# Performance work log

Measured on AMD Instinct MI355X. Metric: run time of the kernel, lower is better.

The kernel has to match this reference:

```python
import jax, jax.numpy as jnp
import numpy as np

HIDDEN = 300
INPUT_DIM = 300


def setup_inputs() -> dict:
    key = jax.random.key(0)
    k_in, k_wih, k_whh, k_bih, k_bhh = jax.random.split(key, 5)
    bound = 1.0 / np.sqrt(HIDDEN)  # PyTorch RNNCell init: U(-1/sqrt(H), 1/sqrt(H))
    inputs = jax.random.normal(k_in, (512, 512, INPUT_DIM), dtype=jnp.float32)
    W_ih = jax.random.uniform(k_wih, (HIDDEN, INPUT_DIM), jnp.float32, -bound, bound)
    W_hh = jax.random.uniform(k_whh, (HIDDEN, HIDDEN), jnp.float32, -bound, bound)
    b_ih = jax.random.uniform(k_bih, (HIDDEN,), jnp.float32, -bound, bound)
    b_hh = jax.random.uniform(k_bhh, (HIDDEN,), jnp.float32, -bound, bound)
    return {"inputs": inputs, "W_ih": W_ih, "W_hh": W_hh, "b_ih": b_ih, "b_hh": b_hh}


def reference(inputs, W_ih, W_hh, b_ih, b_hh):
    # inputs: [seq, batch, input_dim]; vanilla tanh RNNCell scanned over time.
    seq, bz, _ = inputs.shape
    # Precompute input projections for all timesteps in one big GEMM.
    x_proj = jnp.einsum('sbi,hi->sbh', inputs, W_ih) + b_ih + b_hh  # [seq, batch, H]

    def step(ht, xp):
        ht = jnp.tanh(xp + ht @ W_hh.T)
        return ht, None

    h0 = jnp.zeros((bz, HIDDEN), dtype=inputs.dtype)
    ht, _ = jax.lax.scan(step, h0, x_proj)
    return ht
```

## Files before the change

### kernel.cpp

```cpp
#include <hip/hip_runtime.h>
#include <hip/hip_bf16.h>


typedef unsigned short u16;
typedef unsigned int   u32;
typedef __attribute__((ext_vector_type(8)))  short bf16x8;
typedef __attribute__((ext_vector_type(4)))  short s16x4;
typedef __attribute__((ext_vector_type(4)))  float f32x4;
typedef __attribute__((ext_vector_type(16))) float f32x16;
typedef __attribute__((ext_vector_type(2)))  unsigned int u32x2;
typedef __attribute__((ext_vector_type(4)))  unsigned int u32x4;

#define HID 300
#define KP  320
#define SEQ 512
#define BZ  512
#define MTOT (SEQ*BZ)

__device__ __forceinline__ u16 f2bf(float f) {
    u32 u = __float_as_uint(f);
    return (u16)((u + 0x7FFFu + ((u >> 16) & 1u)) >> 16);
}
__device__ __forceinline__ float bf2f(u16 h) {
    return __uint_as_float((u32)h << 16);
}
__device__ __forceinline__ float tanh_fast(float x) {
    float e = __builtin_amdgcn_exp2f(x * 2.8853900817779268f);
    float r = __builtin_amdgcn_rcpf(e + 1.0f);
    return __builtin_fmaf(-2.0f, r, 1.0f);
}
__device__ __forceinline__ u32 pack2(float a, float b) {
    __hip_bfloat162 t = __float22bfloat162_rn(float2{a, b});
    return *(u32*)&t;
}
__device__ __forceinline__ void lds_barrier() {
    asm volatile("s_waitcnt lgkmcnt(0)\n\ts_barrier" ::: "memory");
}

__global__ void prep_kernel(const float* __restrict__ wih,
                            const float* __restrict__ whh,
                            const float* __restrict__ bih,
                            const float* __restrict__ bhh,
                            u16* __restrict__ wihp, u16* __restrict__ whhp,
                            float* __restrict__ bias) {
    int n = blockIdx.x, k = threadIdx.x;
    bool v = (n < HID) && (k < HID);
    int src = n * HID + k, dst = n * KP + k;
    wihp[dst] = v ? f2bf(wih[src]) : (u16)0;
    whhp[dst] = v ? f2bf(whh[src]) : (u16)0;
    if (k == 0) bias[n] = (n < HID) ? (bih[n] + bhh[n]) : 0.0f;
}

__global__ __launch_bounds__(512, 1) void xproj_kernel(
    const float* __restrict__ in, const u16* __restrict__ wihp,
    const float* __restrict__ bias, u16* __restrict__ xp) {
    __shared__ __align__(16) u16 As[2][4096];
    __shared__ __align__(16) u16 Bs[2][10240];

    const int tid = threadIdx.x;
    const int w = tid >> 6, l = tid & 63;
    const int mi = w & 3, ni = w >> 2;
    const int l31 = l & 31, l5 = l >> 5;
    const int m0 = blockIdx.x * 128;

    const int sm = tid >> 2, skg = tid & 3;

    f32x16 acc[5];
#pragma unroll
    for (int j = 0; j < 5; ++j)
#pragma unroll
        for (int r = 0; r < 16; ++r) acc[j][r] = 0.0f;

    auto loadA = [&](int it, f32x4& v0, f32x4& v1) {
        int gk = it * 32 + skg * 8;
        const float* p = in + (size_t)(m0 + sm) * HID + gk;
        if (gk <= 292) { v0 = *(const f32x4*)p; v1 = *(const f32x4*)(p + 4); }
        else if (gk <= 296) { v0 = *(const f32x4*)p; v1 = f32x4{0.f,0.f,0.f,0.f}; }
        else { v0 = f32x4{0.f,0.f,0.f,0.f}; v1 = f32x4{0.f,0.f,0.f,0.f}; }
    };
    auto writeA = [&](int buf, const f32x4& v0, const f32x4& v1) {
        u32x4 pk;
        pk[0] = pack2(v0[0], v0[1]); pk[1] = pack2(v0[2], v0[3]);
        pk[2] = pack2(v1[0], v1[1]); pk[3] = pack2(v1[2], v1[3]);
        *(u32x4*)&As[buf][(skg >> 1) * 2048 + sm * 16 + (skg & 1) * 8] = pk;
    };
    auto stageB = [&](int buf, int it) {
#pragma unroll
        for (int s = 0; s < 3; ++s) {
            int i = w + 8 * s;
            if (i < 20) {
                int c = i & 3, ng = i >> 2;
                int n = ng * 64 + l;
                const u16* g = wihp + n * KP + it * 32 + c * 8;
                u16* d = &Bs[buf][c * 2560 + ng * 512];
                __builtin_amdgcn_global_load_lds(
                    (const __attribute__((address_space(1))) void*)g,
                    (__attribute__((address_space(3))) void*)d, 16, 0, 0);
            }
        }
    };

    {
        f32x4 v0, v1;
        loadA(0, v0, v1);
        writeA(0, v0, v1);
        stageB(0, 0);
    }
    __syncthreads();

#pragma unroll 1
    for (int it = 0; it < 10; ++it) {
        const int cb = it & 1, nb = (it + 1) & 1;
        f32x4 v0, v1;
        if (it < 9) {
            loadA(it + 1, v0, v1);
            stageB(nb, it + 1);
        }
#pragma unroll
        for (int s = 0; s < 2; ++s) {
            bf16x8 a = *(const bf16x8*)&As[cb][s * 2048 + mi * 512 + l31 * 16 + l5 * 8];
#pragma unroll
            for (int j = 0; j < 5; ++j) {
                bf16x8 b = *(const bf16x8*)&Bs[cb][(s * 2 + l5) * 2560 + ((ni * 5 + j) * 32 + l31) * 8];
                acc[j] = __builtin_amdgcn_mfma_f32_32x32x16_bf16(a, b, acc[j], 0, 0, 0);
            }
        }
        if (it < 9) writeA(nb, v0, v1);
        __syncthreads();
    }

    const int mbase = m0 + mi * 32;
#pragma unroll
    for (int j = 0; j < 5; ++j) {
        int n = (ni * 5 + j) * 32 + l31;
        if (n < HID) {
            float bs = bias[n];
#pragma unroll
            for (int reg = 0; reg < 16; ++reg) {
                int row = (reg & 3) + 8 * (reg >> 2) + 4 * l5;
                xp[(size_t)(mbase + row) * HID + n] = f2bf(acc[j][reg] + bs);
            }
        }
    }
}

__global__ __launch_bounds__(512, 2) void rnn_recur_kernel(
    const u16* __restrict__ xp, const u16* __restrict__ whhp,
    float* __restrict__ out) {
    __shared__ __align__(16) u16 hb[2][16 * 328];

    const int tid = threadIdx.x;
    const int w = tid >> 6;
    const int l = tid & 63;
    const int br = l & 15;
    const int q  = l >> 4;
    const int b0 = blockIdx.x * 16;
    const bool t3 = (w < 4);

    for (int i = tid; i < (2 * 16 * 328) / 2; i += 512) ((u32*)hb)[i] = 0;

    bf16x8 Af[3][10];
#pragma unroll
    for (int j = 0; j < 3; ++j) {
        if (j < 2 || t3) {
            const int nt = w + 8 * j;
            const u16* wrow = whhp + (size_t)(nt * 16 + br) * KP;
#pragma unroll
            for (int ks = 0; ks < 10; ++ks)
                Af[j][ks] = *(const bf16x8*)(wrow + ks * 32 + q * 8);
        }
    }
#pragma unroll
    for (int j = 0; j < 3; ++j)
        if (j < 2 || t3)
#pragma unroll
            for (int ks = 0; ks < 10; ++ks)
                asm volatile("" : "+a"(Af[j][ks]));

    int xo[3];
#pragma unroll
    for (int j = 0; j < 3; ++j) {
        int n0 = (w + 8 * j) * 16 + q * 4;
        xo[j] = (n0 < HID && (j < 2 || t3)) ? ((b0 + br) * HID + n0) : -1;
    }

    const s16x4 z4 = {0, 0, 0, 0};
    s16x4 xc[3], xn[3];
#pragma unroll
    for (int j = 0; j < 3; ++j) {
        xc[j] = (xo[j] >= 0) ? *(const s16x4*)(xp + xo[j]) : z4;
        xn[j] = (xo[j] >= 0) ? *(const s16x4*)(xp + (size_t)BZ * HID + xo[j]) : z4;
    }

    lds_barrier();

#pragma unroll 1
    for (int t = 0; t < SEQ; ++t) {
        const u16* hc = hb[t & 1];
        u16*       hn = hb[(t + 1) & 1];

        s16x4 xf[3];
        {
            int t2 = (t + 2 < SEQ) ? (t + 2) : (SEQ - 1);
            const u16* base = xp + (size_t)t2 * (BZ * HID);
#pragma unroll
            for (int j = 0; j < 3; ++j)
                xf[j] = (xo[j] >= 0) ? *(const s16x4*)(base + xo[j]) : z4;
        }

        f32x4 a0, a1, a2;
#pragma unroll
        for (int r = 0; r < 4; ++r) { a0[r] = 0.f; a1[r] = 0.f; a2[r] = 0.f; }

#pragma unroll
        for (int ks = 0; ks < 10; ++ks) {
            bf16x8 bfr = *(const bf16x8*)&hc[br * 328 + ks * 32 + q * 8];
            a0 = __builtin_amdgcn_mfma_f32_16x16x32_bf16(Af[0][ks], bfr, a0, 0, 0, 0);
            a1 = __builtin_amdgcn_mfma_f32_16x16x32_bf16(Af[1][ks], bfr, a1, 0, 0, 0);
            if (t3)
                a2 = __builtin_amdgcn_mfma_f32_16x16x32_bf16(Af[2][ks], bfr, a2, 0, 0, 0);
        }

        {
            int n0 = w * 16 + q * 4;
            u32x2 pk;
            pk[0] = pack2(tanh_fast(a0[0] + bf2f((u16)xc[0][0])),
                          tanh_fast(a0[1] + bf2f((u16)xc[0][1])));
            pk[1] = pack2(tanh_fast(a0[2] + bf2f((u16)xc[0][2])),
                          tanh_fast(a0[3] + bf2f((u16)xc[0][3])));
            *(u32x2*)&hn[br * 328 + n0] = pk;
        }
        {
            int n0 = (w + 8) * 16 + q * 4;
            u32x2 pk;
            pk[0] = pack2(tanh_fast(a1[0] + bf2f((u16)xc[1][0])),
                          tanh_fast(a1[1] + bf2f((u16)xc[1][1])));
            pk[1] = pack2(tanh_fast(a1[2] + bf2f((u16)xc[1][2])),
                          tanh_fast(a1[3] + bf2f((u16)xc[1][3])));
            *(u32x2*)&hn[br * 328 + n0] = pk;
        }
        if (t3) {
            int n0 = (w + 16) * 16 + q * 4;
            u32x2 pk;
            pk[0] = pack2(tanh_fast(a2[0] + bf2f((u16)xc[2][0])),
                          tanh_fast(a2[1] + bf2f((u16)xc[2][1])));
            pk[1] = pack2(tanh_fast(a2[2] + bf2f((u16)xc[2][2])),
                          tanh_fast(a2[3] + bf2f((u16)xc[2][3])));
            *(u32x2*)&hn[br * 328 + n0] = pk;
        }
        lds_barrier();

#pragma unroll
        for (int j = 0; j < 3; ++j) { xc[j] = xn[j]; xn[j] = xf[j]; }
    }

    const u16* hf = hb[0];
    for (int i = tid; i < 16 * HID; i += 512) {
        int r = i / HID, n = i - r * HID;
        out[(size_t)(b0 + r) * HID + n] = bf2f(hf[r * 328 + n]);
    }
}

extern "C" void kernel_launch(void* const* d_in, const int* in_sizes, int n_in,
                              void* d_out, int out_size, void* d_ws, size_t ws_size,
                              hipStream_t stream) {
    const float* in  = (const float*)d_in[0];
    const float* wih = (const float*)d_in[1];
    const float* whh = (const float*)d_in[2];
    const float* bih = (const float*)d_in[3];
    const float* bhh = (const float*)d_in[4];

    char* ws = (char*)d_ws;
    const size_t XP_BYTES = (size_t)MTOT * HID * sizeof(u16);
    u16*   xpb  = (u16*)ws;
    u16*   wihp = (u16*)(ws + XP_BYTES);
    u16*   whhp = (u16*)(ws + XP_BYTES + (size_t)KP * KP * 2);
    float* bias = (float*)(ws + XP_BYTES + 2 * (size_t)KP * KP * 2);

    prep_kernel<<<KP, KP, 0, stream>>>(wih, whh, bih, bhh, wihp, whhp, bias);
    xproj_kernel<<<MTOT / 128, 512, 0, stream>>>(in, wihp, bias, xpb);
    rnn_recur_kernel<<<BZ / 16, 512, 0, stream>>>(xpb, whhp, (float*)d_out);
}
```

Before: 1.091 ms.

## Use 4 waves per block in RNN recurrence with 5 tiles per wave

The recurrent kernel now runs 256 threads (4 waves) per block, and each wave owns 5 output column tiles instead of 2-3. This balances work across waves and makes the per-step barrier cheaper. The accumulators are seeded with the precomputed input projection, which removes the separate add before tanh. The h fragments are loaded once into registers and reused over two MFMA phases, so the first two tiles' tanh and store can overlap the remaining MFMAs. In exchange, each wave has a longer serial chain of MFMAs per timestep and holds more weight fragments in AGPRs.

Result: slower. 1.285 ms (+17.7%).

```diff
diff --git a/kernel.cpp b/kernel.cpp
--- a/kernel.cpp
+++ b/kernel.cpp
@@ -24,8 +24,8 @@
 __device__ __forceinline__ float bf2f(u16 h) {
     return __uint_as_float((u32)h << 16);
 }
-__device__ __forceinline__ float tanh_fast(float x) {
-    float e = __builtin_amdgcn_exp2f(x * 2.8853900817779268f);
+__device__ __forceinline__ float tanh_fast(float y) {
+    float e = __builtin_amdgcn_exp2f(y * 2.8853900817779268f);
     float r = __builtin_amdgcn_rcpf(e + 1.0f);
     return __builtin_fmaf(-2.0f, r, 1.0f);
 }
@@ -144,7 +144,7 @@
     }
 }
 
-__global__ __launch_bounds__(512, 2) void rnn_recur_kernel(
+__global__ __launch_bounds__(256, 1) void rnn_recur_kernel(
     const u16* __restrict__ xp, const u16* __restrict__ whhp,
     float* __restrict__ out) {
     __shared__ __align__(16) u16 hb[2][16 * 328];
@@ -155,39 +155,35 @@
     const int br = l & 15;
     const int q  = l >> 4;
     const int b0 = blockIdx.x * 16;
-    const bool t3 = (w < 4);
-
-    for (int i = tid; i < (2 * 16 * 328) / 2; i += 512) ((u32*)hb)[i] = 0;
-
-    bf16x8 Af[3][10];
-#pragma unroll
-    for (int j = 0; j < 3; ++j) {
-        if (j < 2 || t3) {
-            const int nt = w + 8 * j;
-            const u16* wrow = whhp + (size_t)(nt * 16 + br) * KP;
-#pragma unroll
-            for (int ks = 0; ks < 10; ++ks)
-                Af[j][ks] = *(const bf16x8*)(wrow + ks * 32 + q * 8);
-        }
-    }
-#pragma unroll
-    for (int j = 0; j < 3; ++j)
-        if (j < 2 || t3)
-#pragma unroll
-            for (int ks = 0; ks < 10; ++ks)
-                asm volatile("" : "+a"(Af[j][ks]));
-
-    int xo[3];
-#pragma unroll
-    for (int j = 0; j < 3; ++j) {
-        int n0 = (w + 8 * j) * 16 + q * 4;
-        xo[j] = (n0 < HID && (j < 2 || t3)) ? ((b0 + br) * HID + n0) : -1;
+
+    for (int i = tid; i < (2 * 16 * 328) / 2; i += 256) ((u32*)hb)[i] = 0;
+
+    bf16x8 Af[5][10];
+#pragma unroll
+    for (int j = 0; j < 5; ++j) {
+        const int nt = w + 4 * j;
+        const u16* wrow = whhp + (size_t)(nt * 16 + br) * KP;
+#pragma unroll
+        for (int ks = 0; ks < 10; ++ks)
+            Af[j][ks] = *(const bf16x8*)(wrow + ks * 32 + q * 8);
+    }
+#pragma unroll
+    for (int j = 0; j < 5; ++j)
+#pragma unroll
+        for (int ks = 0; ks < 10; ++ks)
+            asm volatile("" : "+a"(Af[j][ks]));
+
+    int xo[5];
+#pragma unroll
+    for (int j = 0; j < 5; ++j) {
+        int n0 = (w + 4 * j) * 16 + q * 4;
+        xo[j] = (n0 < HID) ? ((b0 + br) * HID + n0) : -1;
     }
 
     const s16x4 z4 = {0, 0, 0, 0};
-    s16x4 xc[3], xn[3];
-#pragma unroll
-    for (int j = 0; j < 3; ++j) {
+    s16x4 xc[5], xn[5];
+#pragma unroll
+    for (int j = 0; j < 5; ++j) {
         xc[j] = (xo[j] >= 0) ? *(const s16x4*)(xp + xo[j]) : z4;
         xn[j] = (xo[j] >= 0) ? *(const s16x4*)(xp + (size_t)BZ * HID + xo[j]) : z4;
     }
@@ -199,63 +195,63 @@
         const u16* hc = hb[t & 1];
         u16*       hn = hb[(t + 1) & 1];
 
-        s16x4 xf[3];
+        s16x4 xf[5];
         {
             int t2 = (t + 2 < SEQ) ? (t + 2) : (SEQ - 1);
             const u16* base = xp + (size_t)t2 * (BZ * HID);
 #pragma unroll
-            for (int j = 0; j < 3; ++j)
+            for (int j = 0; j < 5; ++j)
                 xf[j] = (xo[j] >= 0) ? *(const s16x4*)(base + xo[j]) : z4;
         }
 
-        f32x4 a0, a1, a2;
-#pragma unroll
-        for (int r = 0; r < 4; ++r) { a0[r] = 0.f; a1[r] = 0.f; a2[r] = 0.f; }
-
+        f32x4 a[5];
+#pragma unroll
+        for (int j = 0; j < 5; ++j)
+#pragma unroll
+            for (int r = 0; r < 4; ++r)
+                a[j][r] = bf2f((u16)xc[j][r]);
+
+        bf16x8 bfr[10];
 #pragma unroll
         for (int ks = 0; ks < 10; ++ks) {
-            bf16x8 bfr = *(const bf16x8*)&hc[br * 328 + ks * 32 + q * 8];
-            a0 = __builtin_amdgcn_mfma_f32_16x16x32_bf16(Af[0][ks], bfr, a0, 0, 0, 0);
-            a1 = __builtin_amdgcn_mfma_f32_16x16x32_bf16(Af[1][ks], bfr, a1, 0, 0, 0);
-            if (t3)
-                a2 = __builtin_amdgcn_mfma_f32_16x16x32_bf16(Af[2][ks], bfr, a2, 0, 0, 0);
-        }
-
-        {
-            int n0 = w * 16 + q * 4;
+            bfr[ks] = *(const bf16x8*)&hc[br * 328 + ks * 32 + q * 8];
+            a[0] = __builtin_amdgcn_mfma_f32_16x16x32_bf16(Af[0][ks], bfr[ks], a[0], 0, 0, 0);
+            a[1] = __builtin_amdgcn_mfma_f32_16x16x32_bf16(Af[1][ks], bfr[ks], a[1], 0, 0, 0);
+        }
+
+#pragma unroll
+        for (int j = 0; j < 2; ++j) {
+            int n0 = (w + 4 * j) * 16 + q * 4;
             u32x2 pk;
-            pk[0] = pack2(tanh_fast(a0[0] + bf2f((u16)xc[0][0])),
-                          tanh_fast(a0[1] + bf2f((u16)xc[0][1])));
-            pk[1] = pack2(tanh_fast(a0[2] + bf2f((u16)xc[0][2])),
-                          tanh_fast(a0[3] + bf2f((u16)xc[0][3])));
+            pk[0] = pack2(tanh_fast(a[j][0]), tanh_fast(a[j][1]));
+            pk[1] = pack2(tanh_fast(a[j][2]), tanh_fast(a[j][3]));
             *(u32x2*)&hn[br * 328 + n0] = pk;
         }
-        {
-            int n0 = (w + 8) * 16 + q * 4;
+
+#pragma unroll
+        for (int ks = 0; ks < 10; ++ks) {
+            a[2] = __builtin_amdgcn_mfma_f32_16x16x32_bf16(Af[2][ks], bfr[ks], a[2], 0, 0, 0);
+            a[3] = __builtin_amdgcn_mfma_f32_16x16x32_bf16(Af[3][ks], bfr[ks], a[3], 0, 0, 0);
+            a[4] = __builtin_amdgcn_mfma_f32_16x16x32_bf16(Af[4][ks], bfr[ks], a[4], 0, 0, 0);
+        }
+
+#pragma unroll
+        for (int j = 2; j < 5; ++j) {
+            int n0 = (w + 4 * j) * 16 + q * 4;
             u32x2 pk;
-            pk[0] = pack2(tanh_fast(a1[0] + bf2f((u16)xc[1][0])),
-                          tanh_fast(a1[1] + bf2f((u16)xc[1][1])));
-            pk[1] = pack2(tanh_fast(a1[2] + bf2f((u16)xc[1][2])),
-                          tanh_fast(a1[3] + bf2f((u16)xc[1][3])));
+            pk[0] = pack2(tanh_fast(a[j][0]), tanh_fast(a[j][1]));
+            pk[1] = pack2(tanh_fast(a[j][2]), tanh_fast(a[j][3]));
             *(u32x2*)&hn[br * 328 + n0] = pk;
         }
-        if (t3) {
-            int n0 = (w + 16) * 16 + q * 4;
-            u32x2 pk;
-            pk[0] = pack2(tanh_fast(a2[0] + bf2f((u16)xc[2][0])),
-                          tanh_fast(a2[1] + bf2f((u16)xc[2][1])));
-            pk[1] = pack2(tanh_fast(a2[2] + bf2f((u16)xc[2][2])),
-                          tanh_fast(a2[3] + bf2f((u16)xc[2][3])));
-            *(u32x2*)&hn[br * 328 + n0] = pk;
-        }
+
         lds_barrier();
 
 #pragma unroll
-        for (int j = 0; j < 3; ++j) { xc[j] = xn[j]; xn[j] = xf[j]; }
+        for (int j = 0; j < 5; ++j) { xc[j] = xn[j]; xn[j] = xf[j]; }
     }
 
     const u16* hf = hb[0];
-    for (int i = tid; i < 16 * HID; i += 512) {
+    for (int i = tid; i < 16 * HID; i += 256) {
         int r = i / HID, n = i - r * HID;
         out[(size_t)(b0 + r) * HID + n] = bf2f(hf[r * 328 + n]);
     }
@@ -279,5 +275,5 @@
 
     prep_kernel<<<KP, KP, 0, stream>>>(wih, whh, bih, bhh, wihp, whhp, bias);
     xproj_kernel<<<MTOT / 128, 512, 0, stream>>>(in, wihp, bias, xpb);
-    rnn_recur_kernel<<<BZ / 16, 512, 0, stream>>>(xpb, whhp, (float*)d_out);
-}
+    rnn_recur_kernel<<<BZ / 16, 256, 0, stream>>>(xpb, whhp, (float*)d_out);
+}
```

## Load xproj GEMM fragments directly from global into registers, drop LDS staging

Applied to the files above, without the earlier changes.

The input-projection GEMM no longer stages A and B tiles through shared memory. Each wave now loads its MFMA fragments straight from global memory into registers, software-pipelined one step ahead, with K stepped in chunks of 16 instead of 32. Each wave computes a 64x160 tile with two accumulator sets, and blocks shrink to 256 threads so two can share a CU. This removes the LDS writes, reads and barriers, at the cost of uncoalesced strided global loads and redundant reloads of the weights across waves, plus higher register pressure.

Measured after the change: 1.204 ms. +10.3%, slower.

```diff
diff --git a/kernel.cpp b/kernel.cpp
--- a/kernel.cpp
+++ b/kernel.cpp
@@ -51,94 +51,89 @@
     if (k == 0) bias[n] = (n < HID) ? (bih[n] + bhh[n]) : 0.0f;
 }
 
-__global__ __launch_bounds__(512, 1) void xproj_kernel(
+__global__ __launch_bounds__(256, 2) void xproj_kernel(
     const float* __restrict__ in, const u16* __restrict__ wihp,
     const float* __restrict__ bias, u16* __restrict__ xp) {
-    __shared__ __align__(16) u16 As[2][4096];
-    __shared__ __align__(16) u16 Bs[2][10240];
-
     const int tid = threadIdx.x;
-    const int w = tid >> 6, l = tid & 63;
-    const int mi = w & 3, ni = w >> 2;
+    const int w   = tid >> 6;
+    const int l   = tid & 63;
     const int l31 = l & 31, l5 = l >> 5;
-    const int m0 = blockIdx.x * 128;
-
-    const int sm = tid >> 2, skg = tid & 3;
-
-    f32x16 acc[5];
+    const int mi  = w & 1, ni = w >> 1;
+    const int m0  = blockIdx.x * 128 + mi * 64;
+
+    const int aoff0 = (m0 + l31) * HID + l5 * 8;
+    const int aoff1 = aoff0 + 32 * HID;
+    int boff[5];
 #pragma unroll
     for (int j = 0; j < 5; ++j)
-#pragma unroll
-        for (int r = 0; r < 16; ++r) acc[j][r] = 0.0f;
-
-    auto loadA = [&](int it, f32x4& v0, f32x4& v1) {
-        int gk = it * 32 + skg * 8;
-        const float* p = in + (size_t)(m0 + sm) * HID + gk;
-        if (gk <= 292) { v0 = *(const f32x4*)p; v1 = *(const f32x4*)(p + 4); }
-        else if (gk <= 296) { v0 = *(const f32x4*)p; v1 = f32x4{0.f,0.f,0.f,0.f}; }
-        else { v0 = f32x4{0.f,0.f,0.f,0.f}; v1 = f32x4{0.f,0.f,0.f,0.f}; }
+        boff[j] = ((ni * 5 + j) * 32 + l31) * KP + l5 * 8;
+
+    f32x16 acc0[5], acc1[5];
+#pragma unroll
+    for (int j = 0; j < 5; ++j)
+#pragma unroll
+        for (int r = 0; r < 16; ++r) { acc0[j][r] = 0.0f; acc1[j][r] = 0.0f; }
+
+    auto mkfrag = [](const f32x4& u0, const f32x4& u1) -> bf16x8 {
+        union { u32x4 u; bf16x8 b; } cv;
+        cv.u[0] = pack2(u0[0], u0[1]); cv.u[1] = pack2(u0[2], u0[3]);
+        cv.u[2] = pack2(u1[0], u1[1]); cv.u[3] = pack2(u1[2], u1[3]);
+        return cv.b;
     };
-    auto writeA = [&](int buf, const f32x4& v0, const f32x4& v1) {
-        u32x4 pk;
-        pk[0] = pack2(v0[0], v0[1]); pk[1] = pack2(v0[2], v0[3]);
-        pk[2] = pack2(v1[0], v1[1]); pk[3] = pack2(v1[2], v1[3]);
-        *(u32x4*)&As[buf][(skg >> 1) * 2048 + sm * 16 + (skg & 1) * 8] = pk;
+    const f32x4 zf = {0.f, 0.f, 0.f, 0.f};
+
+    auto loadA = [&](int it, bf16x8& A0, bf16x8& A1, bool last) {
+        const float* p0 = in + aoff0 + it * 16;
+        const float* p1 = in + aoff1 + it * 16;
+        f32x4 u0 = *(const f32x4*)p0;
+        f32x4 w0 = *(const f32x4*)p1;
+        f32x4 u1, w1;
+        if (last && l5 == 1) { u1 = zf; w1 = zf; }
+        else { u1 = *(const f32x4*)(p0 + 4); w1 = *(const f32x4*)(p1 + 4); }
+        A0 = mkfrag(u0, u1);
+        A1 = mkfrag(w0, w1);
     };
-    auto stageB = [&](int buf, int it) {
-#pragma unroll
-        for (int s = 0; s < 3; ++s) {
-            int i = w + 8 * s;
-            if (i < 20) {
-                int c = i & 3, ng = i >> 2;
-                int n = ng * 64 + l;
-                const u16* g = wihp + n * KP + it * 32 + c * 8;
-                u16* d = &Bs[buf][c * 2560 + ng * 512];
-                __builtin_amdgcn_global_load_lds(
-                    (const __attribute__((address_space(1))) void*)g,
-                    (__attribute__((address_space(3))) void*)d, 16, 0, 0);
-            }
-        }
+    auto loadB = [&](int it, bf16x8* B) {
+#pragma unroll
+        for (int j = 0; j < 5; ++j)
+            B[j] = *(const bf16x8*)(wihp + boff[j] + it * 16);
     };
 
-    {
-        f32x4 v0, v1;
-        loadA(0, v0, v1);
-        writeA(0, v0, v1);
-        stageB(0, 0);
-    }
-    __syncthreads();
+    bf16x8 A0c, A1c, Bc[5];
+    loadA(0, A0c, A1c, false);
+    loadB(0, Bc);
 
 #pragma unroll 1
-    for (int it = 0; it < 10; ++it) {
-        const int cb = it & 1, nb = (it + 1) & 1;
-        f32x4 v0, v1;
-        if (it < 9) {
-            loadA(it + 1, v0, v1);
-            stageB(nb, it + 1);
-        }
-#pragma unroll
-        for (int s = 0; s < 2; ++s) {
-            bf16x8 a = *(const bf16x8*)&As[cb][s * 2048 + mi * 512 + l31 * 16 + l5 * 8];
-#pragma unroll
-            for (int j = 0; j < 5; ++j) {
-                bf16x8 b = *(const bf16x8*)&Bs[cb][(s * 2 + l5) * 2560 + ((ni * 5 + j) * 32 + l31) * 8];
-                acc[j] = __builtin_amdgcn_mfma_f32_32x32x16_bf16(a, b, acc[j], 0, 0, 0);
-            }
-        }
-        if (it < 9) writeA(nb, v0, v1);
-        __syncthreads();
-    }
-
-    const int mbase = m0 + mi * 32;
+    for (int it = 0; it < 18; ++it) {
+        bf16x8 A0n, A1n, Bn[5];
+        loadA(it + 1, A0n, A1n, it + 1 == 18);
+        loadB(it + 1, Bn);
+#pragma unroll
+        for (int j = 0; j < 5; ++j) {
+            acc0[j] = __builtin_amdgcn_mfma_f32_32x32x16_bf16(A0c, Bc[j], acc0[j], 0, 0, 0);
+            acc1[j] = __builtin_amdgcn_mfma_f32_32x32x16_bf16(A1c, Bc[j], acc1[j], 0, 0, 0);
+        }
+        A0c = A0n; A1c = A1n;
+#pragma unroll
+        for (int j = 0; j < 5; ++j) Bc[j] = Bn[j];
+    }
+#pragma unroll
+    for (int j = 0; j < 5; ++j) {
+        acc0[j] = __builtin_amdgcn_mfma_f32_32x32x16_bf16(A0c, Bc[j], acc0[j], 0, 0, 0);
+        acc1[j] = __builtin_amdgcn_mfma_f32_32x32x16_bf16(A1c, Bc[j], acc1[j], 0, 0, 0);
+    }
+
 #pragma unroll
     for (int j = 0; j < 5; ++j) {
         int n = (ni * 5 + j) * 32 + l31;
         if (n < HID) {
             float bs = bias[n];
+            int rbase = m0 + 4 * l5;
 #pragma unroll
             for (int reg = 0; reg < 16; ++reg) {
-                int row = (reg & 3) + 8 * (reg >> 2) + 4 * l5;
-                xp[(size_t)(mbase + row) * HID + n] = f2bf(acc[j][reg] + bs);
+                int row = rbase + (reg & 3) + 8 * (reg >> 2);
+                xp[(size_t)row * HID + n] = f2bf(acc0[j][reg] + bs);
+                xp[(size_t)(row + 32) * HID + n] = f2bf(acc1[j][reg] + bs);
             }
         }
     }
@@ -278,6 +273,6 @@
     float* bias = (float*)(ws + XP_BYTES + 2 * (size_t)KP * KP * 2);
 
     prep_kernel<<<KP, KP, 0, stream>>>(wih, whh, bih, bhh, wihp, whhp, bias);
-    xproj_kernel<<<MTOT / 128, 512, 0, stream>>>(in, wihp, bias, xpb);
+    xproj_kernel<<<MTOT / 128, 256, 0, stream>>>(in, wihp, bias, xpb);
     rnn_recur_kernel<<<BZ / 16, 512, 0, stream>>>(xpb, whhp, (float*)d_out);
 }
```

## Triple-buffer weight tiles in xproj GEMM and split recurrence into two launches

Applied to the files above, without the earlier changes.

The xproj GEMM now keeps three LDS buffers for the weight tiles, issuing async global-to-LDS loads two iterations ahead. Explicit vmcnt waits plus an LDS barrier replace the full __syncthreads. The A-tile loads become branchless, using clamped addresses and selects. The recurrence kernel is split into two launches over half the sequence each, with the bf16 hidden state passed through the output buffer; this adds launch and state-transfer overhead with no clear gain.

After: 1.093 ms. No clear change (+0.2%).

```diff
diff --git a/kernel.cpp b/kernel.cpp
--- a/kernel.cpp
+++ b/kernel.cpp
@@ -55,7 +55,7 @@
     const float* __restrict__ in, const u16* __restrict__ wihp,
     const float* __restrict__ bias, u16* __restrict__ xp) {
     __shared__ __align__(16) u16 As[2][4096];
-    __shared__ __align__(16) u16 Bs[2][10240];
+    __shared__ __align__(16) u16 Bs[3][10240];
 
     const int tid = threadIdx.x;
     const int w = tid >> 6, l = tid & 63;
@@ -71,12 +71,16 @@
 #pragma unroll
         for (int r = 0; r < 16; ++r) acc[j][r] = 0.0f;
 
+    const f32x4 zf = {0.f, 0.f, 0.f, 0.f};
     auto loadA = [&](int it, f32x4& v0, f32x4& v1) {
         int gk = it * 32 + skg * 8;
-        const float* p = in + (size_t)(m0 + sm) * HID + gk;
-        if (gk <= 292) { v0 = *(const f32x4*)p; v1 = *(const f32x4*)(p + 4); }
-        else if (gk <= 296) { v0 = *(const f32x4*)p; v1 = f32x4{0.f,0.f,0.f,0.f}; }
-        else { v0 = f32x4{0.f,0.f,0.f,0.f}; v1 = f32x4{0.f,0.f,0.f,0.f}; }
+        int a0 = gk > 296 ? 296 : gk;
+        int a1 = (gk + 4) > 296 ? 296 : (gk + 4);
+        const float* p = in + (size_t)(m0 + sm) * HID;
+        v0 = *(const f32x4*)(p + a0);
+        v1 = *(const f32x4*)(p + a1);
+        v0 = (gk > 296) ? zf : v0;
+        v1 = ((gk + 4) > 296) ? zf : v1;
     };
     auto writeA = [&](int buf, const f32x4& v0, const f32x4& v1) {
         u32x4 pk;
@@ -101,32 +105,39 @@
     };
 
     {
+        stageB(0, 0);
         f32x4 v0, v1;
         loadA(0, v0, v1);
         writeA(0, v0, v1);
-        stageB(0, 0);
-    }
-    __syncthreads();
-
+        stageB(1, 1);
+        asm volatile("s_waitcnt vmcnt(2)" ::: "memory");
+        lds_barrier();
+    }
+
+    int cA = 0, cB = 0, sB = 2;
 #pragma unroll 1
     for (int it = 0; it < 10; ++it) {
-        const int cb = it & 1, nb = (it + 1) & 1;
         f32x4 v0, v1;
-        if (it < 9) {
-            loadA(it + 1, v0, v1);
-            stageB(nb, it + 1);
-        }
+        if (it < 9) loadA(it + 1, v0, v1);
+        if (it < 8) stageB(sB, it + 2);
 #pragma unroll
         for (int s = 0; s < 2; ++s) {
-            bf16x8 a = *(const bf16x8*)&As[cb][s * 2048 + mi * 512 + l31 * 16 + l5 * 8];
+            bf16x8 a = *(const bf16x8*)&As[cA][s * 2048 + mi * 512 + l31 * 16 + l5 * 8];
 #pragma unroll
             for (int j = 0; j < 5; ++j) {
-                bf16x8 b = *(const bf16x8*)&Bs[cb][(s * 2 + l5) * 2560 + ((ni * 5 + j) * 32 + l31) * 8];
+                bf16x8 b = *(const bf16x8*)&Bs[cB][(s * 2 + l5) * 2560 + ((ni * 5 + j) * 32 + l31) * 8];
                 acc[j] = __builtin_amdgcn_mfma_f32_32x32x16_bf16(a, b, acc[j], 0, 0, 0);
             }
         }
-        if (it < 9) writeA(nb, v0, v1);
-        __syncthreads();
+        if (it < 9) {
+            writeA(cA ^ 1, v0, v1);
+            if (it < 8) asm volatile("s_waitcnt vmcnt(3)" ::: "memory");
+            else        asm volatile("s_waitcnt vmcnt(2)" ::: "memory");
+            lds_barrier();
+        }
+        cA ^= 1;
+        cB = (cB == 2) ? 0 : cB + 1;
+        sB = (sB == 2) ? 0 : sB + 1;
     }
 
     const int mbase = m0 + mi * 32;
@@ -146,7 +157,7 @@
 
 __global__ __launch_bounds__(512, 2) void rnn_recur_kernel(
     const u16* __restrict__ xp, const u16* __restrict__ whhp,
-    float* __restrict__ out) {
+    float* __restrict__ out, int t0, int t1) {
     __shared__ __align__(16) u16 hb[2][16 * 328];
 
     const int tid = threadIdx.x;
@@ -177,6 +188,15 @@
             for (int ks = 0; ks < 10; ++ks)
                 asm volatile("" : "+a"(Af[j][ks]));
 
+    lds_barrier();
+    if (t0 > 0) {
+        const u16* hs = (const u16*)out;
+        for (int i = tid; i < 16 * HID; i += 512) {
+            int r = i / HID, n = i - r * HID;
+            hb[0][r * 328 + n] = hs[(size_t)(b0 + r) * HID + n];
+        }
+    }
+
     int xo[3];
 #pragma unroll
     for (int j = 0; j < 3; ++j) {
@@ -188,14 +208,14 @@
     s16x4 xc[3], xn[3];
 #pragma unroll
     for (int j = 0; j < 3; ++j) {
-        xc[j] = (xo[j] >= 0) ? *(const s16x4*)(xp + xo[j]) : z4;
-        xn[j] = (xo[j] >= 0) ? *(const s16x4*)(xp + (size_t)BZ * HID + xo[j]) : z4;
+        xc[j] = (xo[j] >= 0) ? *(const s16x4*)(xp + (size_t)t0 * (BZ * HID) + xo[j]) : z4;
+        xn[j] = (xo[j] >= 0) ? *(const s16x4*)(xp + (size_t)(t0 + 1) * (BZ * HID) + xo[j]) : z4;
     }
 
     lds_barrier();
 
 #pragma unroll 1
-    for (int t = 0; t < SEQ; ++t) {
+    for (int t = t0; t < t1; ++t) {
         const u16* hc = hb[t & 1];
         u16*       hn = hb[(t + 1) & 1];
 
@@ -255,9 +275,17 @@
     }
 
     const u16* hf = hb[0];
-    for (int i = tid; i < 16 * HID; i += 512) {
-        int r = i / HID, n = i - r * HID;
-        out[(size_t)(b0 + r) * HID + n] = bf2f(hf[r * 328 + n]);
+    if (t1 == SEQ) {
+        for (int i = tid; i < 16 * HID; i += 512) {
+            int r = i / HID, n = i - r * HID;
+            out[(size_t)(b0 + r) * HID + n] = bf2f(hf[r * 328 + n]);
+        }
+    } else {
+        u16* hs = (u16*)out;
+        for (int i = tid; i < 16 * HID; i += 512) {
+            int r = i / HID, n = i - r * HID;
+            hs[(size_t)(b0 + r) * HID + n] = hf[r * 328 + n];
+        }
     }
 }
 
@@ -279,5 +307,6 @@
 
     prep_kernel<<<KP, KP, 0, stream>>>(wih, whh, bih, bhh, wihp, whhp, bias);
     xproj_kernel<<<MTOT / 128, 512, 0, stream>>>(in, wihp, bias, xpb);
-    rnn_recur_kernel<<<BZ / 16, 512, 0, stream>>>(xpb, whhp, (float*)d_out);
-}
+    rnn_recur_kernel<<<BZ / 16, 512, 0, stream>>>(xpb, whhp, (float*)d_out, 0, SEQ / 2);
+    rnn_recur_kernel<<<BZ / 16, 512, 0, stream>>>(xpb, whhp, (float*)d_out, SEQ / 2, SEQ);
+}
```
